# Kernel optimization log

Hardware: AMD Instinct MI355X
Metric: run time of the kernel (lower is better)

## Reference

```python
import jax, jax.numpy as jnp
import numpy as np

N_PAPER, N_MESH = 60000, 30000
N = N_PAPER + N_MESH
E_TRAIN, E_DEC = 2000000, 400000
F_PAPER = F_MESH = 128
D0, H, D = 16, 32, 16  # initial embed, hidden, final embed
NREL, NB = 2, 4


def _glorot(key, shape):
    fan_in, fan_out = shape[-2], shape[-1]
    s = jnp.sqrt(6.0 / (fan_in + fan_out)).astype(jnp.float32)
    return jax.random.uniform(key, shape, jnp.float32, -s, s)


def setup_inputs() -> dict:
    key = jax.random.key(0)
    ks = iter(jax.random.split(key, 40))
    inp = {
        'x_paper': jax.random.normal(next(ks), (N_PAPER, F_PAPER), jnp.float32),
        'x_mesh': jax.random.normal(next(ks), (N_MESH, F_MESH), jnp.float32),
        'train_edge_index': jax.random.randint(next(ks), (2, E_TRAIN), 0, N, jnp.int64 if jax.config.jax_enable_x64 else jnp.int32),
        'train_edge_type': jnp.sort(jax.random.randint(next(ks), (E_TRAIN,), 0, NREL)),
        'pos_edge_index': jax.random.randint(next(ks), (2, E_DEC), 0, N),
        'pos_edge_type': jnp.sort(jax.random.randint(next(ks), (E_DEC,), 0, NREL)),
        'neg_edge_index': jax.random.randint(next(ks), (2, E_DEC), 0, N),
        'neg_edge_type': jnp.sort(jax.random.randint(next(ks), (E_DEC,), 0, NREL)),
        # input transforms
        'Wp': _glorot(next(ks), (F_PAPER, D0)), 'bp': jnp.zeros((D0,), jnp.float32),
        'Wm': _glorot(next(ks), (F_MESH, D0)), 'bm': jnp.zeros((D0,), jnp.float32),
        # decode linears
        'Wd0': _glorot(next(ks), (D, D)), 'bd0': jnp.zeros((D,), jnp.float32),
        'Wd1': _glorot(next(ks), (D, D)), 'bd1': jnp.zeros((D,), jnp.float32),
    }
    dims = [(D0, H), (H, H), (H, H), (H, D)]
    for i, (di, do) in enumerate(dims, 1):
        inp[f'bases{i}'] = _glorot(next(ks), (NB, di, do))
        inp[f'comp{i}'] = _glorot(next(ks), (NREL, NB))
        inp[f'root{i}'] = _glorot(next(ks), (di, do))
        inp[f'bias{i}'] = jnp.zeros((do,), jnp.float32)
    return inp


def rgcn_layer(x, src, dst, et, bases, comp, root, bias):
    # PyG RGCNConv with basis decomposition, per-relation mean aggregation.
    out = x @ root + bias
    xs = x[src]  # [E, in]
    for r in range(NREL):
        W_r = jnp.einsum('b,bio->io', comp[r], bases)
        m = xs @ W_r  # [E, out]
        mf = (et == r).astype(m.dtype)
        cnt = jax.ops.segment_sum(mf, dst, num_segments=N)
        agg = jax.ops.segment_sum(m * mf[:, None], dst, num_segments=N)
        out = out + agg / jnp.clip(cnt, 1.0)[:, None]
    return out


def _decode_block(z, ei, et, Wd0, bd0, Wd1, bd1):
    zs, zd = z[ei[0]], z[ei[1]]
    h0 = zs @ Wd0 + bd0
    h1 = zs @ Wd1 + bd1
    h = jnp.where((et == 0)[:, None], h0, h1)
    return jnp.sum(h * zd, axis=-1)


def reference(x_paper, x_mesh, train_edge_index, train_edge_type,
              pos_edge_index, pos_edge_type, neg_edge_index, neg_edge_type,
              Wp, bp, Wm, bm, Wd0, bd0, Wd1, bd1,
              bases1, comp1, root1, bias1, bases2, comp2, root2, bias2,
              bases3, comp3, root3, bias3, bases4, comp4, root4, bias4):
    x = jnp.concatenate([x_paper @ Wp + bp, x_mesh @ Wm + bm], axis=0)  # [N, D0]
    src, dst = train_edge_index[0], train_edge_index[1]
    x = jax.nn.relu(rgcn_layer(x, src, dst, train_edge_type, bases1, comp1, root1, bias1))
    x = jax.nn.relu(rgcn_layer(x, src, dst, train_edge_type, bases2, comp2, root2, bias2))
    x = jax.nn.relu(rgcn_layer(x, src, dst, train_edge_type, bases3, comp3, root3, bias3))
    z = rgcn_layer(x, src, dst, train_edge_type, bases4, comp4, root4, bias4)
    # edge types are sorted, so per-edge in-order compute matches the masked concat order
    pos = _decode_block(z, pos_edge_index, pos_edge_type, Wd0, bd0, Wd1, bd1)
    neg = _decode_block(z, neg_edge_index, neg_edge_type, Wd0, bd0, Wd1, bd1)
    return jnp.concatenate([pos, neg], axis=0)  # [2*E_DEC]
```

## Files before the change

kernel.cpp:

```cpp
#include <hip/hip_runtime.h>
#include <hip/hip_bf16.h>

constexpr int NN = 90000;
constexpr int NP = 60000;
constexpr int NM = 30000;
constexpr int ET = 2000000;
constexpr int ED = 400000;
constexpr int TWO_NN = 2 * NN;

constexpr int BKT_SH  = 9;
constexpr int NB_BKT  = (TWO_NN + 511) >> BKT_SH;
constexpr int BKT_CAP = 6400;
constexpr int TILE    = 2048;
constexpr int N_TILES = (ET + TILE - 1) / TILE;

__device__ __forceinline__ float bflo(unsigned int u) {
    union { unsigned int i; float f; } c;
    c.i = u << 16;
    return c.f;
}
__device__ __forceinline__ float bfhi(unsigned int u) {
    union { unsigned int i; float f; } c;
    c.i = u & 0xffff0000u;
    return c.f;
}
__device__ __forceinline__ unsigned short f2bf(float f) {
    union { float f; unsigned int i; } c;
    c.f = f;
    unsigned int x = c.i;
    return (unsigned short)((x + 0x7FFFu + ((x >> 16) & 1u)) >> 16);
}

__global__ void init_kernel(const int* __restrict__ tei, int* __restrict__ gcur,
                            int* __restrict__ dflag) {
    int b = blockIdx.x * blockDim.x + threadIdx.x;
    if (b < NB_BKT) gcur[b] = b * BKT_CAP;
    if (b == 0) {
        int allzero = 1;
        for (int i = 0; i < 16; i++)
            if (tei[2 * i + 1] != 0) allzero = 0;
        dflag[0] = allzero;
    }
}

__global__ void __launch_bounds__(256) binA_kernel(
        const int* __restrict__ ei, const int* __restrict__ et,
        const int* __restrict__ dflag, int* __restrict__ gcur,
        int2* __restrict__ pairs) {
    __shared__ int histw[4][NB_BKT];
    __shared__ int wbase[4][NB_BKT];
    __shared__ int tot[NB_BKT];
    __shared__ int excl[NB_BKT];
    __shared__ int gbase[NB_BKT];
    __shared__ int scn[256];
    __shared__ int2 tbuf[TILE];
    int t = threadIdx.x;
    int w = t >> 6;
    int tile0 = blockIdx.x * TILE;
    int tcount = ET - tile0;
    if (tcount > TILE) tcount = TILE;
    for (int i = t; i < 4 * NB_BKT; i += 256) ((int*)histw)[i] = 0;
    __syncthreads();
    int sft = dflag[0];
    int myk[8], mys[8];
#pragma unroll
    for (int q = 0; q < 8; q++) {
        int li = q * 256 + t;
        myk[q] = -1;
        if (li < tcount) {
            int e = tile0 + li;
            int s = ei[(size_t)e << sft];
            int d = ei[(size_t)(ET + e) << sft];
            int r = et[(size_t)e << sft];
            int key = r * NN + d;
            myk[q] = key;
            mys[q] = s;
            atomicAdd(&histw[w][key >> BKT_SH], 1);
        }
    }
    __syncthreads();
    for (int i = t; i < NB_BKT; i += 256) {
        int h0 = histw[0][i], h1 = histw[1][i], h2 = histw[2][i], h3 = histw[3][i];
        wbase[0][i] = 0;
        wbase[1][i] = h0;
        wbase[2][i] = h0 + h1;
        wbase[3][i] = h0 + h1 + h2;
        tot[i] = h0 + h1 + h2 + h3;
    }
    __syncthreads();
    int v0 = (t < NB_BKT / 2) ? tot[2 * t] : 0;
    int v1 = (t < NB_BKT / 2) ? tot[2 * t + 1] : 0;
    int s = v0 + v1;
    scn[t] = s;
    __syncthreads();
    for (int st = 1; st < 256; st <<= 1) {
        int u = (t >= st) ? scn[t - st] : 0;
        __syncthreads();
        scn[t] += u;
        __syncthreads();
    }
    int base = scn[t] - s;
    if (t < NB_BKT / 2) {
        excl[2 * t] = base;
        excl[2 * t + 1] = base + v0;
    }
    __syncthreads();
    for (int i = t; i < NB_BKT; i += 256) {
        int e0 = excl[i];
        wbase[0][i] += e0;
        wbase[1][i] += e0;
        wbase[2][i] += e0;
        wbase[3][i] += e0;
        histw[0][i] = 0; histw[1][i] = 0; histw[2][i] = 0; histw[3][i] = 0;
    }
    __syncthreads();
#pragma unroll
    for (int q = 0; q < 8; q++) {
        if (myk[q] >= 0) {
            int b = myk[q] >> BKT_SH;
            int p = wbase[w][b] + atomicAdd(&histw[w][b], 1);
            tbuf[p] = make_int2(myk[q], mys[q]);
        }
    }
    __syncthreads();
    for (int i = t; i < NB_BKT; i += 256)
        if (tot[i] > 0) gbase[i] = atomicAdd(&gcur[i], tot[i]);
    __syncthreads();
    for (int i = t; i < tcount; i += 256) {
        int2 p = tbuf[i];
        int b = p.x >> BKT_SH;
        int gpos = gbase[b] + (i - excl[b]);
        int cap = (b + 1) * BKT_CAP - 1;
        pairs[gpos < cap ? gpos : cap] = p;
    }
}

__global__ void __launch_bounds__(256) histplace_kernel(
        const int* __restrict__ gcur, const int2* __restrict__ pairs,
        int* __restrict__ off, int* __restrict__ endo, float* __restrict__ inv,
        int* __restrict__ csr) {
    __shared__ int kh[512];
    __shared__ int scn[256];
    int b = blockIdx.x;
    int t = threadIdx.x;
    int beg = b * BKT_CAP, end = gcur[b];
    for (int i = t; i < 512; i += 256) kh[i] = 0;
    __syncthreads();
    for (int i = beg + t; i < end; i += 256)
        atomicAdd(&kh[pairs[i].x & 511], 1);
    __syncthreads();
    int v[2];
    int s = 0;
#pragma unroll
    for (int q = 0; q < 2; q++) {
        v[q] = kh[t * 2 + q];
        s += v[q];
    }
    scn[t] = s;
    __syncthreads();
    for (int st = 1; st < 256; st <<= 1) {
        int u = (t >= st) ? scn[t - st] : 0;
        __syncthreads();
        scn[t] += u;
        __syncthreads();
    }
    int run = beg + scn[t] - s;
    int kbase = b << BKT_SH;
    int kc[2];
#pragma unroll
    for (int q = 0; q < 2; q++) {
        int key = kbase + t * 2 + q;
        if (key < TWO_NN) {
            off[key] = run;
            endo[key] = run + v[q];
            inv[key] = 1.0f / (float)(v[q] > 1 ? v[q] : 1);
        }
        kc[q] = run;
        run += v[q];
    }
    __syncthreads();
#pragma unroll
    for (int q = 0; q < 2; q++) kh[t * 2 + q] = kc[q];
    __syncthreads();
    for (int i = beg + t; i < end; i += 256) {
        int2 p = pairs[i];
        int pos = atomicAdd(&kh[p.x & 511], 1);
        csr[pos] = p.y;
    }
}

__global__ void __launch_bounds__(256) embed2_kernel(
        const float* __restrict__ Xp, const float* __restrict__ Xm,
        const float* __restrict__ Wp, const float* __restrict__ bp,
        const float* __restrict__ Wm, const float* __restrict__ bm,
        unsigned short* __restrict__ outbf) {
    __shared__ float Wl[4096 + 32];
    for (int i = threadIdx.x; i < 2048; i += 256) {
        Wl[i] = Wp[i];
        Wl[2048 + i] = Wm[i];
    }
    if (threadIdx.x < 16) {
        Wl[4096 + threadIdx.x] = bp[threadIdx.x];
        Wl[4112 + threadIdx.x] = bm[threadIdx.x];
    }
    __syncthreads();
    int n = blockIdx.x * 256 + threadIdx.x;
    if (n >= NN) return;
    const float* X;
    const float* Ws;
    const float* Bs;
    if (n < NP) { X = Xp + (size_t)n * 128; Ws = Wl; Bs = Wl + 4096; }
    else        { X = Xm + (size_t)(n - NP) * 128; Ws = Wl + 2048; Bs = Wl + 4112; }
    float acc[16];
#pragma unroll
    for (int j = 0; j < 16; j++) acc[j] = Bs[j];
    const float4* row = (const float4*)X;
    for (int k4 = 0; k4 < 32; k4++) {
        float4 xv = row[k4];
        int k = k4 * 4;
#pragma unroll
        for (int j = 0; j < 16; j++) {
            float a = acc[j];
            a = fmaf(xv.x, Ws[(k + 0) * 16 + j], a);
            a = fmaf(xv.y, Ws[(k + 1) * 16 + j], a);
            a = fmaf(xv.z, Ws[(k + 2) * 16 + j], a);
            a = fmaf(xv.w, Ws[(k + 3) * 16 + j], a);
            acc[j] = a;
        }
    }
    ushort4* ob = (ushort4*)(outbf + (size_t)n * 16);
#pragma unroll
    for (int q = 0; q < 4; q++) {
        ushort4 ub;
        ub.x = f2bf(acc[4 * q]);     ub.y = f2bf(acc[4 * q + 1]);
        ub.z = f2bf(acc[4 * q + 2]); ub.w = f2bf(acc[4 * q + 3]);
        ob[q] = ub;
    }
}

__global__ void prep_all_kernel(
        const float* __restrict__ ba0, const float* __restrict__ co0,
        const float* __restrict__ ro0, const float* __restrict__ bi0,
        const float* __restrict__ ba1, const float* __restrict__ co1,
        const float* __restrict__ ro1, const float* __restrict__ bi1,
        const float* __restrict__ ba2, const float* __restrict__ co2,
        const float* __restrict__ ro2, const float* __restrict__ bi2,
        const float* __restrict__ ba3, const float* __restrict__ co3,
        const float* __restrict__ ro3, const float* __restrict__ bi3,
        float* __restrict__ Wbuf4) {
    int l = blockIdx.x;
    const float* bases; const float* comp; const float* root; const float* bias;
    if (l == 0)      { bases = ba0; comp = co0; root = ro0; bias = bi0; }
    else if (l == 1) { bases = ba1; comp = co1; root = ro1; bias = bi1; }
    else if (l == 2) { bases = ba2; comp = co2; root = ro2; bias = bi2; }
    else             { bases = ba3; comp = co3; root = ro3; bias = bi3; }
    int din = (l == 0) ? 16 : 32;
    int dout = (l == 3) ? 16 : 32;
    int sz = din * dout;
    float* W = Wbuf4 + l * 3200;
    for (int i = threadIdx.x; i < sz; i += 256) {
        float b0 = bases[i];
        float b1 = bases[sz + i];
        float b2 = bases[2 * sz + i];
        float b3 = bases[3 * sz + i];
        for (int r = 0; r < 2; r++) {
            W[r * sz + i] = comp[r * 4 + 0] * b0 + comp[r * 4 + 1] * b1 +
                            comp[r * 4 + 2] * b2 + comp[r * 4 + 3] * b3;
        }
        W[2 * sz + i] = root[i];
    }
    if (threadIdx.x < dout) W[3 * sz + threadIdx.x] = bias[threadIdx.x];
}

template <int DIN, int DOUT, int RELU>
__global__ void __launch_bounds__(256) layer_kernel(
        const int* __restrict__ off, const int* __restrict__ endo,
        const int* __restrict__ csr,
        const unsigned short* __restrict__ xbf_in,
        const float* __restrict__ inv, const float* __restrict__ Wbuf,
        unsigned short* __restrict__ xbf_out) {
    constexpr int SZ = DIN * DOUT;
    constexpr int QL = DIN / 8;
    constexpr int TPN = 2 * QL;
    constexpr int NPB = 256 / TPN;
    constexpr int AGST = 2 * DIN + 4;
    constexpr int XSST = DIN + 4;
    __shared__ float Wl[3 * SZ + DOUT];
    __shared__ float agg[NPB * AGST];
    __shared__ float xs[NPB * XSST];
    for (int i = threadIdx.x; i < 3 * SZ + DOUT; i += 256) Wl[i] = Wbuf[i];
    int t = threadIdx.x;
    int ln = t / TPN;
    int rl = t % TPN;
    int r = rl / QL;
    int lane = rl % QL;
    int d = blockIdx.x * NPB + ln;
    if (d < NN) {
        if (r == 0) {
            uint4 u = *(const uint4*)(xbf_in + (size_t)d * DIN + lane * 8);
            float* xp = xs + ln * XSST + lane * 8;
            xp[0] = bflo(u.x); xp[1] = bfhi(u.x);
            xp[2] = bflo(u.y); xp[3] = bfhi(u.y);
            xp[4] = bflo(u.z); xp[5] = bfhi(u.z);
            xp[6] = bflo(u.w); xp[7] = bfhi(u.w);
        }
        int key = r * NN + d;
        int b = off[key];
        int e = endo[key];
        float a0[8] = {0, 0, 0, 0, 0, 0, 0, 0};
        float a1[8] = {0, 0, 0, 0, 0, 0, 0, 0};
        const unsigned short* hp = xbf_in + lane * 8;
        int k = b;
        for (; k + 1 < e; k += 2) {
            int s0 = csr[k];
            int s1 = csr[k + 1];
            uint4 u0 = *(const uint4*)(hp + (size_t)s0 * DIN);
            uint4 u1 = *(const uint4*)(hp + (size_t)s1 * DIN);
            a0[0] += bflo(u0.x); a0[1] += bfhi(u0.x);
            a0[2] += bflo(u0.y); a0[3] += bfhi(u0.y);
            a0[4] += bflo(u0.z); a0[5] += bfhi(u0.z);
            a0[6] += bflo(u0.w); a0[7] += bfhi(u0.w);
            a1[0] += bflo(u1.x); a1[1] += bfhi(u1.x);
            a1[2] += bflo(u1.y); a1[3] += bfhi(u1.y);
            a1[4] += bflo(u1.z); a1[5] += bfhi(u1.z);
            a1[6] += bflo(u1.w); a1[7] += bfhi(u1.w);
        }
        if (k < e) {
            uint4 u0 = *(const uint4*)(hp + (size_t)csr[k] * DIN);
            a0[0] += bflo(u0.x); a0[1] += bfhi(u0.x);
            a0[2] += bflo(u0.y); a0[3] += bfhi(u0.y);
            a0[4] += bflo(u0.z); a0[5] += bfhi(u0.z);
            a0[6] += bflo(u0.w); a0[7] += bfhi(u0.w);
        }
        float* ap = agg + ln * AGST + r * DIN + lane * 8;
        *(float4*)ap = make_float4(a0[0] + a1[0], a0[1] + a1[1],
                                   a0[2] + a1[2], a0[3] + a1[3]);
        *(float4*)(ap + 4) = make_float4(a0[4] + a1[4], a0[5] + a1[5],
                                         a0[6] + a1[6], a0[7] + a1[7]);
    }
    __syncthreads();
    constexpr int CPN = DOUT / 4;
    for (int tt = t; tt < NPB * CPN; tt += 256) {
        int ln2 = tt / CPN;
        int j0 = (tt % CPN) * 4;
        int d2 = blockIdx.x * NPB + ln2;
        if (d2 < NN) {
            float iv0 = inv[d2], iv1 = inv[NN + d2];
            float acc[4];
#pragma unroll
            for (int jj = 0; jj < 4; jj++) acc[jj] = Wl[3 * SZ + j0 + jj];
#pragma unroll
            for (int k = 0; k < DIN; k++) {
                float xv = xs[ln2 * XSST + k];
                float m0 = agg[ln2 * AGST + k] * iv0;
                float m1 = agg[ln2 * AGST + DIN + k] * iv1;
                const float* w0 = &Wl[k * DOUT + j0];
                const float* w1 = &Wl[SZ + k * DOUT + j0];
                const float* wr = &Wl[2 * SZ + k * DOUT + j0];
#pragma unroll
                for (int jj = 0; jj < 4; jj++) {
                    acc[jj] = fmaf(xv, wr[jj], acc[jj]);
                    acc[jj] = fmaf(m0, w0[jj], acc[jj]);
                    acc[jj] = fmaf(m1, w1[jj], acc[jj]);
                }
            }
            if (RELU) {
#pragma unroll
                for (int jj = 0; jj < 4; jj++) acc[jj] = fmaxf(acc[jj], 0.0f);
            }
            ushort4 ub;
            ub.x = f2bf(acc[0]); ub.y = f2bf(acc[1]);
            ub.z = f2bf(acc[2]); ub.w = f2bf(acc[3]);
            *(ushort4*)(xbf_out + (size_t)d2 * DOUT + j0) = ub;
        }
    }
}

__global__ void __launch_bounds__(256) decode_fused_kernel(
        const unsigned short* __restrict__ zbf,
        const float* __restrict__ Wd0, const float* __restrict__ bd0,
        const float* __restrict__ Wd1, const float* __restrict__ bd1,
        const int* __restrict__ pei, const int* __restrict__ pet,
        const int* __restrict__ nei, const int* __restrict__ net_,
        float* __restrict__ out, const int* __restrict__ dflag) {
    __shared__ float W[2][256];
    __shared__ float B[2][16];
    for (int i = threadIdx.x; i < 256; i += 256) {
        W[0][i] = Wd0[i];
        W[1][i] = Wd1[i];
    }
    if (threadIdx.x < 16) {
        B[0][threadIdx.x] = bd0[threadIdx.x];
        B[1][threadIdx.x] = bd1[threadIdx.x];
    }
    __syncthreads();
    int i = blockIdx.x * 256 + threadIdx.x;
    if (i >= 2 * ED) return;
    int sft = dflag[0];
    const int* ei;
    const int* et;
    int e;
    if (i < ED) { ei = pei; et = pet; e = i; }
    else        { ei = nei; et = net_; e = i - ED; }
    int s = ei[(size_t)e << sft];
    int d = ei[(size_t)(ED + e) << sft];
    int r = et[(size_t)e << sft];
    float zs[16], zd[16];
    const uint4* sp = (const uint4*)(zbf + ((size_t)s << 4));
    const uint4* dp = (const uint4*)(zbf + ((size_t)d << 4));
#pragma unroll
    for (int h = 0; h < 2; h++) {
        uint4 us = sp[h];
        uint4 ud = dp[h];
        int o8 = h * 8;
        zs[o8 + 0] = bflo(us.x); zs[o8 + 1] = bfhi(us.x);
        zs[o8 + 2] = bflo(us.y); zs[o8 + 3] = bfhi(us.y);
        zs[o8 + 4] = bflo(us.z); zs[o8 + 5] = bfhi(us.z);
        zs[o8 + 6] = bflo(us.w); zs[o8 + 7] = bfhi(us.w);
        zd[o8 + 0] = bflo(ud.x); zd[o8 + 1] = bfhi(ud.x);
        zd[o8 + 2] = bflo(ud.y); zd[o8 + 3] = bfhi(ud.y);
        zd[o8 + 4] = bflo(ud.z); zd[o8 + 5] = bfhi(ud.z);
        zd[o8 + 6] = bflo(ud.w); zd[o8 + 7] = bfhi(ud.w);
    }
    const float* Wr = W[r];
    const float* Br = B[r];
    float acc = 0.0f;
#pragma unroll
    for (int j = 0; j < 16; j++) {
        float yj = Br[j];
#pragma unroll
        for (int k = 0; k < 16; k++) yj = fmaf(zs[k], Wr[k * 16 + j], yj);
        acc = fmaf(yj, zd[j], acc);
    }
    out[i] = acc;
}

extern "C" void kernel_launch(void* const* d_in, const int* in_sizes, int n_in,
                              void* d_out, int out_size, void* d_ws, size_t ws_size,
                              hipStream_t stream) {
    const float* x_paper = (const float*)d_in[0];
    const float* x_mesh  = (const float*)d_in[1];
    const int* tei  = (const int*)d_in[2];
    const int* tet  = (const int*)d_in[3];
    const int* pei  = (const int*)d_in[4];
    const int* pet  = (const int*)d_in[5];
    const int* nei  = (const int*)d_in[6];
    const int* net_ = (const int*)d_in[7];
    const float* Wp  = (const float*)d_in[8];
    const float* bp  = (const float*)d_in[9];
    const float* Wm  = (const float*)d_in[10];
    const float* bm  = (const float*)d_in[11];
    const float* Wd0 = (const float*)d_in[12];
    const float* bd0 = (const float*)d_in[13];
    const float* Wd1 = (const float*)d_in[14];
    const float* bd1 = (const float*)d_in[15];

    float* ws = (float*)d_ws;
    size_t o = 0;
    unsigned short* xbfA = (unsigned short*)(ws + o); o += (size_t)NN * 16;
    unsigned short* xbfB = (unsigned short*)(ws + o); o += (size_t)NN * 16;
    float* inv  = ws + o; o += (size_t)TWO_NN;
    int*   off  = (int*)(ws + o); o += (size_t)TWO_NN;
    int*   endo = (int*)(ws + o); o += (size_t)TWO_NN;
    int*   csr  = (int*)(ws + o); o += (size_t)NB_BKT * BKT_CAP;
    int*   gcur = (int*)(ws + o); o += 512;
    int2*  pairs = (int2*)(ws + o); o += (size_t)2 * NB_BKT * BKT_CAP;
    float* Wbuf4 = ws + o; o += 4 * 3200;
    int*   dflag = (int*)(ws + o); o += 16;

    init_kernel<<<(NB_BKT + 255) / 256, 256, 0, stream>>>(tei, gcur, dflag);

    binA_kernel<<<N_TILES, 256, 0, stream>>>(tei, tet, dflag, gcur, pairs);
    histplace_kernel<<<NB_BKT, 256, 0, stream>>>(gcur, pairs, off, endo, inv, csr);

    embed2_kernel<<<(NN + 255) / 256, 256, 0, stream>>>(
        x_paper, x_mesh, Wp, bp, Wm, bm, xbfA);

    prep_all_kernel<<<4, 256, 0, stream>>>(
        (const float*)d_in[16], (const float*)d_in[17], (const float*)d_in[18], (const float*)d_in[19],
        (const float*)d_in[20], (const float*)d_in[21], (const float*)d_in[22], (const float*)d_in[23],
        (const float*)d_in[24], (const float*)d_in[25], (const float*)d_in[26], (const float*)d_in[27],
        (const float*)d_in[28], (const float*)d_in[29], (const float*)d_in[30], (const float*)d_in[31],
        Wbuf4);

    int blk16 = (NN + 63) / 64;
    int blk32 = (NN + 31) / 32;
    layer_kernel<16, 32, 1><<<blk16, 256, 0, stream>>>(
        off, endo, csr, xbfA, inv, Wbuf4 + 0 * 3200, xbfB);
    layer_kernel<32, 32, 1><<<blk32, 256, 0, stream>>>(
        off, endo, csr, xbfB, inv, Wbuf4 + 1 * 3200, xbfA);
    layer_kernel<32, 32, 1><<<blk32, 256, 0, stream>>>(
        off, endo, csr, xbfA, inv, Wbuf4 + 2 * 3200, xbfB);
    layer_kernel<32, 16, 0><<<blk32, 256, 0, stream>>>(
        off, endo, csr, xbfB, inv, Wbuf4 + 3 * 3200, xbfA);

    decode_fused_kernel<<<(2 * ED + 255) / 256, 256, 0, stream>>>(
        xbfA, Wd0, bd0, Wd1, bd1, pei, pet, nei, net_, (float*)d_out, dflag);
}
```

Before: 372.3 us.

## Split node features into column slices and separate gather from combine

Node features are stored as two column slices, each holding half the feature width. Each layer is split into a gather kernel that sums neighbour slices into a global fp32 aggregation buffer and a combine kernel that applies the weight matrices. The aim is a smaller gather working set per pass, so random neighbour reads hit in cache more often, with block ordering interleaving the two slices. The cost is an extra fp32 round trip to global memory for the aggregates and twice as many kernel launches; the pairs buffer is aliased onto the aggregation buffer.

```diff
diff --git a/kernel.cpp b/kernel.cpp
--- a/kernel.cpp
+++ b/kernel.cpp
@@ -193,7 +193,7 @@
         const float* __restrict__ Xp, const float* __restrict__ Xm,
         const float* __restrict__ Wp, const float* __restrict__ bp,
         const float* __restrict__ Wm, const float* __restrict__ bm,
-        unsigned short* __restrict__ outbf) {
+        unsigned short* __restrict__ xc) {
     __shared__ float Wl[4096 + 32];
     for (int i = threadIdx.x; i < 2048; i += 256) {
         Wl[i] = Wp[i];
@@ -228,13 +228,16 @@
             acc[j] = a;
         }
     }
-    ushort4* ob = (ushort4*)(outbf + (size_t)n * 16);
-#pragma unroll
-    for (int q = 0; q < 4; q++) {
-        ushort4 ub;
-        ub.x = f2bf(acc[4 * q]);     ub.y = f2bf(acc[4 * q + 1]);
-        ub.z = f2bf(acc[4 * q + 2]); ub.w = f2bf(acc[4 * q + 3]);
-        ob[q] = ub;
+#pragma unroll
+    for (int sl = 0; sl < 2; sl++) {
+        ushort4 u0, u1;
+        u0.x = f2bf(acc[sl * 8 + 0]); u0.y = f2bf(acc[sl * 8 + 1]);
+        u0.z = f2bf(acc[sl * 8 + 2]); u0.w = f2bf(acc[sl * 8 + 3]);
+        u1.x = f2bf(acc[sl * 8 + 4]); u1.y = f2bf(acc[sl * 8 + 5]);
+        u1.z = f2bf(acc[sl * 8 + 6]); u1.w = f2bf(acc[sl * 8 + 7]);
+        unsigned short* p = xc + ((size_t)sl * NN + n) * 8;
+        *(ushort4*)p = u0;
+        *(ushort4*)(p + 4) = u1;
     }
 }
 
@@ -272,107 +275,140 @@
     if (threadIdx.x < dout) W[3 * sz + threadIdx.x] = bias[threadIdx.x];
 }
 
-template <int DIN, int DOUT, int RELU>
-__global__ void __launch_bounds__(256) layer_kernel(
+template <int DIN>
+__global__ void __launch_bounds__(256) gather_slice_kernel(
         const int* __restrict__ off, const int* __restrict__ endo,
-        const int* __restrict__ csr,
-        const unsigned short* __restrict__ xbf_in,
+        const int* __restrict__ csr, const unsigned short* __restrict__ xc,
+        float* __restrict__ agg) {
+    constexpr int F = DIN / 2;
+    constexpr int LPS = F / 8;
+    constexpr int GPB = 256 / LPS;
+    int b = blockIdx.x;
+    int slice = (b & 7) >> 2;
+    int kb = (b >> 3) * 4 + (b & 3);
+    int gi = kb * GPB + (int)threadIdx.x / LPS;
+    if (gi >= TWO_NN) return;
+    int lane = (int)threadIdx.x % LPS;
+    const unsigned short* hp = xc + (size_t)slice * NN * F + lane * 8;
+    int beg = off[gi], end = endo[gi];
+    float a0[8] = {0, 0, 0, 0, 0, 0, 0, 0};
+    float a1[8] = {0, 0, 0, 0, 0, 0, 0, 0};
+    int k = beg;
+    for (; k + 1 < end; k += 2) {
+        int s0 = csr[k];
+        int s1 = csr[k + 1];
+        uint4 u0 = *(const uint4*)(hp + (size_t)s0 * F);
+        uint4 u1 = *(const uint4*)(hp + (size_t)s1 * F);
+        a0[0] += bflo(u0.x); a0[1] += bfhi(u0.x);
+        a0[2] += bflo(u0.y); a0[3] += bfhi(u0.y);
+        a0[4] += bflo(u0.z); a0[5] += bfhi(u0.z);
+        a0[6] += bflo(u0.w); a0[7] += bfhi(u0.w);
+        a1[0] += bflo(u1.x); a1[1] += bfhi(u1.x);
+        a1[2] += bflo(u1.y); a1[3] += bfhi(u1.y);
+        a1[4] += bflo(u1.z); a1[5] += bfhi(u1.z);
+        a1[6] += bflo(u1.w); a1[7] += bfhi(u1.w);
+    }
+    if (k < end) {
+        uint4 u0 = *(const uint4*)(hp + (size_t)csr[k] * F);
+        a0[0] += bflo(u0.x); a0[1] += bfhi(u0.x);
+        a0[2] += bflo(u0.y); a0[3] += bfhi(u0.y);
+        a0[4] += bflo(u0.z); a0[5] += bfhi(u0.z);
+        a0[6] += bflo(u0.w); a0[7] += bfhi(u0.w);
+    }
+    int rel = gi >= NN ? 1 : 0;
+    int d = gi - rel * NN;
+    float* ap = agg + (((size_t)slice * 2 + rel) * NN + d) * F + lane * 8;
+    *(float4*)ap = make_float4(a0[0] + a1[0], a0[1] + a1[1],
+                               a0[2] + a1[2], a0[3] + a1[3]);
+    *(float4*)(ap + 4) = make_float4(a0[4] + a1[4], a0[5] + a1[5],
+                                     a0[6] + a1[6], a0[7] + a1[7]);
+}
+
+template <int DIN, int DOUT, int RELU, int ZOUT>
+__global__ void __launch_bounds__(256) combine_kernel(
+        const unsigned short* __restrict__ xc_in, const float* __restrict__ agg,
         const float* __restrict__ inv, const float* __restrict__ Wbuf,
-        unsigned short* __restrict__ xbf_out) {
+        unsigned short* __restrict__ xc_out) {
+    constexpr int F = DIN / 2;
     constexpr int SZ = DIN * DOUT;
-    constexpr int QL = DIN / 8;
-    constexpr int TPN = 2 * QL;
-    constexpr int NPB = 256 / TPN;
+    constexpr int CPN = DOUT / 4;
+    constexpr int NPB = 256 / CPN;
+    constexpr int XSST = DIN + 4;
     constexpr int AGST = 2 * DIN + 4;
-    constexpr int XSST = DIN + 4;
     __shared__ float Wl[3 * SZ + DOUT];
-    __shared__ float agg[NPB * AGST];
     __shared__ float xs[NPB * XSST];
-    for (int i = threadIdx.x; i < 3 * SZ + DOUT; i += 256) Wl[i] = Wbuf[i];
+    __shared__ float ag[NPB * AGST];
     int t = threadIdx.x;
-    int ln = t / TPN;
-    int rl = t % TPN;
-    int r = rl / QL;
-    int lane = rl % QL;
-    int d = blockIdx.x * NPB + ln;
-    if (d < NN) {
-        if (r == 0) {
-            uint4 u = *(const uint4*)(xbf_in + (size_t)d * DIN + lane * 8);
-            float* xp = xs + ln * XSST + lane * 8;
+    for (int i = t; i < 3 * SZ + DOUT; i += 256) Wl[i] = Wbuf[i];
+    int n0 = blockIdx.x * NPB;
+    constexpr int CH = DIN / 8;
+    for (int i = t; i < NPB * CH; i += 256) {
+        int node = i / CH, c = i % CH;
+        int n = n0 + node;
+        if (n < NN) {
+            int slice = c / (F / 8);
+            int cc = c % (F / 8);
+            uint4 u = *(const uint4*)(xc_in + ((size_t)slice * NN + n) * F + cc * 8);
+            float* xp = xs + node * XSST + slice * F + cc * 8;
             xp[0] = bflo(u.x); xp[1] = bfhi(u.x);
             xp[2] = bflo(u.y); xp[3] = bfhi(u.y);
             xp[4] = bflo(u.z); xp[5] = bfhi(u.z);
             xp[6] = bflo(u.w); xp[7] = bfhi(u.w);
         }
-        int key = r * NN + d;
-        int b = off[key];
-        int e = endo[key];
-        float a0[8] = {0, 0, 0, 0, 0, 0, 0, 0};
-        float a1[8] = {0, 0, 0, 0, 0, 0, 0, 0};
-        const unsigned short* hp = xbf_in + lane * 8;
-        int k = b;
-        for (; k + 1 < e; k += 2) {
-            int s0 = csr[k];
-            int s1 = csr[k + 1];
-            uint4 u0 = *(const uint4*)(hp + (size_t)s0 * DIN);
-            uint4 u1 = *(const uint4*)(hp + (size_t)s1 * DIN);
-            a0[0] += bflo(u0.x); a0[1] += bfhi(u0.x);
-            a0[2] += bflo(u0.y); a0[3] += bfhi(u0.y);
-            a0[4] += bflo(u0.z); a0[5] += bfhi(u0.z);
-            a0[6] += bflo(u0.w); a0[7] += bfhi(u0.w);
-            a1[0] += bflo(u1.x); a1[1] += bfhi(u1.x);
-            a1[2] += bflo(u1.y); a1[3] += bfhi(u1.y);
-            a1[4] += bflo(u1.z); a1[5] += bfhi(u1.z);
-            a1[6] += bflo(u1.w); a1[7] += bfhi(u1.w);
-        }
-        if (k < e) {
-            uint4 u0 = *(const uint4*)(hp + (size_t)csr[k] * DIN);
-            a0[0] += bflo(u0.x); a0[1] += bfhi(u0.x);
-            a0[2] += bflo(u0.y); a0[3] += bfhi(u0.y);
-            a0[4] += bflo(u0.z); a0[5] += bfhi(u0.z);
-            a0[6] += bflo(u0.w); a0[7] += bfhi(u0.w);
-        }
-        float* ap = agg + ln * AGST + r * DIN + lane * 8;
-        *(float4*)ap = make_float4(a0[0] + a1[0], a0[1] + a1[1],
-                                   a0[2] + a1[2], a0[3] + a1[3]);
-        *(float4*)(ap + 4) = make_float4(a0[4] + a1[4], a0[5] + a1[5],
-                                         a0[6] + a1[6], a0[7] + a1[7]);
-    }
-    __syncthreads();
-    constexpr int CPN = DOUT / 4;
-    for (int tt = t; tt < NPB * CPN; tt += 256) {
-        int ln2 = tt / CPN;
-        int j0 = (tt % CPN) * 4;
-        int d2 = blockIdx.x * NPB + ln2;
-        if (d2 < NN) {
-            float iv0 = inv[d2], iv1 = inv[NN + d2];
-            float acc[4];
-#pragma unroll
-            for (int jj = 0; jj < 4; jj++) acc[jj] = Wl[3 * SZ + j0 + jj];
-#pragma unroll
-            for (int k = 0; k < DIN; k++) {
-                float xv = xs[ln2 * XSST + k];
-                float m0 = agg[ln2 * AGST + k] * iv0;
-                float m1 = agg[ln2 * AGST + DIN + k] * iv1;
-                const float* w0 = &Wl[k * DOUT + j0];
-                const float* w1 = &Wl[SZ + k * DOUT + j0];
-                const float* wr = &Wl[2 * SZ + k * DOUT + j0];
-#pragma unroll
-                for (int jj = 0; jj < 4; jj++) {
-                    acc[jj] = fmaf(xv, wr[jj], acc[jj]);
-                    acc[jj] = fmaf(m0, w0[jj], acc[jj]);
-                    acc[jj] = fmaf(m1, w1[jj], acc[jj]);
-                }
-            }
-            if (RELU) {
-#pragma unroll
-                for (int jj = 0; jj < 4; jj++) acc[jj] = fmaxf(acc[jj], 0.0f);
-            }
-            ushort4 ub;
-            ub.x = f2bf(acc[0]); ub.y = f2bf(acc[1]);
-            ub.z = f2bf(acc[2]); ub.w = f2bf(acc[3]);
-            *(ushort4*)(xbf_out + (size_t)d2 * DOUT + j0) = ub;
-        }
+    }
+    constexpr int QPR = F / 4;
+    constexpr int CH2 = 2 * DIN / 4;
+    for (int i = t; i < NPB * CH2; i += 256) {
+        int node = i / CH2, c = i % CH2;
+        int n = n0 + node;
+        if (n < NN) {
+            int slice = c / (2 * QPR);
+            int rem = c % (2 * QPR);
+            int rel = rem / QPR;
+            int q = rem % QPR;
+            float4 v = *(const float4*)(
+                agg + (((size_t)slice * 2 + rel) * NN + n) * F + q * 4);
+            float* gp = ag + node * AGST + rel * DIN + slice * F + q * 4;
+            gp[0] = v.x; gp[1] = v.y; gp[2] = v.z; gp[3] = v.w;
+        }
+    }
+    __syncthreads();
+    int node = t / CPN;
+    int j0 = (t % CPN) * 4;
+    int d2 = n0 + node;
+    if (d2 >= NN) return;
+    float iv0 = inv[d2], iv1 = inv[NN + d2];
+    float acc[4];
+#pragma unroll
+    for (int jj = 0; jj < 4; jj++) acc[jj] = Wl[3 * SZ + j0 + jj];
+#pragma unroll
+    for (int k = 0; k < DIN; k++) {
+        float xv = xs[node * XSST + k];
+        float m0 = ag[node * AGST + k] * iv0;
+        float m1 = ag[node * AGST + DIN + k] * iv1;
+        const float* w0 = &Wl[k * DOUT + j0];
+        const float* w1 = &Wl[SZ + k * DOUT + j0];
+        const float* wr = &Wl[2 * SZ + k * DOUT + j0];
+#pragma unroll
+        for (int jj = 0; jj < 4; jj++) {
+            acc[jj] = fmaf(xv, wr[jj], acc[jj]);
+            acc[jj] = fmaf(m0, w0[jj], acc[jj]);
+            acc[jj] = fmaf(m1, w1[jj], acc[jj]);
+        }
+    }
+    if (RELU) {
+#pragma unroll
+        for (int jj = 0; jj < 4; jj++) acc[jj] = fmaxf(acc[jj], 0.0f);
+    }
+    ushort4 ub;
+    ub.x = f2bf(acc[0]); ub.y = f2bf(acc[1]);
+    ub.z = f2bf(acc[2]); ub.w = f2bf(acc[3]);
+    if (ZOUT) {
+        *(ushort4*)(xc_out + (size_t)d2 * DOUT + j0) = ub;
+    } else {
+        constexpr int FO = DOUT / 2;
+        int so = j0 >= FO ? 1 : 0;
+        *(ushort4*)(xc_out + ((size_t)so * NN + d2) * FO + (j0 - so * FO)) = ub;
     }
 }
 
@@ -457,16 +493,18 @@
 
     float* ws = (float*)d_ws;
     size_t o = 0;
-    unsigned short* xbfA = (unsigned short*)(ws + o); o += (size_t)NN * 16;
-    unsigned short* xbfB = (unsigned short*)(ws + o); o += (size_t)NN * 16;
+    float* aggbuf = ws + o; o += (size_t)NN * 64;
+    unsigned short* xcA = (unsigned short*)(ws + o); o += (size_t)NN * 16;
+    unsigned short* xcB = (unsigned short*)(ws + o); o += (size_t)NN * 16;
+    unsigned short* zbf = (unsigned short*)(ws + o); o += (size_t)NN * 8;
     float* inv  = ws + o; o += (size_t)TWO_NN;
     int*   off  = (int*)(ws + o); o += (size_t)TWO_NN;
     int*   endo = (int*)(ws + o); o += (size_t)TWO_NN;
     int*   csr  = (int*)(ws + o); o += (size_t)NB_BKT * BKT_CAP;
     int*   gcur = (int*)(ws + o); o += 512;
-    int2*  pairs = (int2*)(ws + o); o += (size_t)2 * NB_BKT * BKT_CAP;
     float* Wbuf4 = ws + o; o += 4 * 3200;
     int*   dflag = (int*)(ws + o); o += 16;
+    int2*  pairs = (int2*)aggbuf;
 
     init_kernel<<<(NB_BKT + 255) / 256, 256, 0, stream>>>(tei, gcur, dflag);
 
@@ -474,7 +512,7 @@
     histplace_kernel<<<NB_BKT, 256, 0, stream>>>(gcur, pairs, off, endo, inv, csr);
 
     embed2_kernel<<<(NN + 255) / 256, 256, 0, stream>>>(
-        x_paper, x_mesh, Wp, bp, Wm, bm, xbfA);
+        x_paper, x_mesh, Wp, bp, Wm, bm, xcA);
 
     prep_all_kernel<<<4, 256, 0, stream>>>(
         (const float*)d_in[16], (const float*)d_in[17], (const float*)d_in[18], (const float*)d_in[19],
@@ -483,17 +521,24 @@
         (const float*)d_in[28], (const float*)d_in[29], (const float*)d_in[30], (const float*)d_in[31],
         Wbuf4);
 
-    int blk16 = (NN + 63) / 64;
-    int blk32 = (NN + 31) / 32;
-    layer_kernel<16, 32, 1><<<blk16, 256, 0, stream>>>(
-        off, endo, csr, xbfA, inv, Wbuf4 + 0 * 3200, xbfB);
-    layer_kernel<32, 32, 1><<<blk32, 256, 0, stream>>>(
-        off, endo, csr, xbfB, inv, Wbuf4 + 1 * 3200, xbfA);
-    layer_kernel<32, 32, 1><<<blk32, 256, 0, stream>>>(
-        off, endo, csr, xbfA, inv, Wbuf4 + 2 * 3200, xbfB);
-    layer_kernel<32, 16, 0><<<blk32, 256, 0, stream>>>(
-        off, endo, csr, xbfB, inv, Wbuf4 + 3 * 3200, xbfA);
+    int g16 = 8 * (((TWO_NN + 255) / 256 + 3) / 4);
+    int g32 = 8 * (((TWO_NN + 127) / 128 + 3) / 4);
+    int c32 = (NN + 31) / 32;
+    int c16 = (NN + 63) / 64;
+
+    gather_slice_kernel<16><<<g16, 256, 0, stream>>>(off, endo, csr, xcA, aggbuf);
+    combine_kernel<16, 32, 1, 0><<<c32, 256, 0, stream>>>(xcA, aggbuf, inv,
+                                                          Wbuf4 + 0 * 3200, xcB);
+    gather_slice_kernel<32><<<g32, 256, 0, stream>>>(off, endo, csr, xcB, aggbuf);
+    combine_kernel<32, 32, 1, 0><<<c32, 256, 0, stream>>>(xcB, aggbuf, inv,
+                                                          Wbuf4 + 1 * 3200, xcA);
+    gather_slice_kernel<32><<<g32, 256, 0, stream>>>(off, endo, csr, xcA, aggbuf);
+    combine_kernel<32, 32, 1, 0><<<c32, 256, 0, stream>>>(xcA, aggbuf, inv,
+                                                          Wbuf4 + 2 * 3200, xcB);
+    gather_slice_kernel<32><<<g32, 256, 0, stream>>>(off, endo, csr, xcB, aggbuf);
+    combine_kernel<32, 16, 0, 1><<<c16, 256, 0, stream>>>(xcB, aggbuf, inv,
+                                                          Wbuf4 + 3 * 3200, zbf);
 
     decode_fused_kernel<<<(2 * ED + 255) / 256, 256, 0, stream>>>(
-        xbfA, Wd0, bd0, Wd1, bd1, pei, pet, nei, net_, (float*)d_out, dflag);
-}
+        zbf, Wd0, bd0, Wd1, bd1, pei, pet, nei, net_, (float*)d_out, dflag);
+}
```

Result: slower. 438.5 us (+17.8%).
